# Performance work log

Hardware: AMD Instinct MI355X
Metric: run time of the kernel (lower is better)

The kernel has to match this reference:

```python
import jax, jax.numpy as jnp
import numpy as np

FEATHER = (16, 16)          # in_feather_size
OUT_FEATHER = (16, 16)      # out_feather_size
F = FEATHER[0] * FEATHER[1]            # 256
INNER = (F + 1) ** 2                   # 66049
OUT = OUT_FEATHER[0] * OUT_FEATHER[1]  # 256
B = 2048


def setup_inputs() -> dict:
    key = jax.random.key(0)
    kx, kw, kb = jax.random.split(key, 3)
    x = jax.random.normal(kx, (B, F), dtype=jnp.float32)
    # nn.Linear(INNER, OUT): weight [OUT, INNER], bias [OUT]
    bound = 1.0 / np.sqrt(INNER)
    W = jax.random.uniform(kw, (OUT, INNER), dtype=jnp.float32, minval=-bound, maxval=bound)
    b = jax.random.uniform(kb, (OUT,), dtype=jnp.float32, minval=-bound, maxval=bound)
    return {"x": x, "W": W, "b": b}


def reference(x, W, b):
    # x: [B, F] -> prepend 1 -> x1: [B, F+1]
    x = x.reshape(-1, F)
    ones = jnp.ones((x.shape[0], 1), dtype=x.dtype)
    x1 = jnp.concatenate([ones, x], axis=-1)          # [B, F+1]
    # batched outer product, flattened: [B, (F+1)^2]
    outer = (x1[:, :, None] * x1[:, None, :]).reshape(x.shape[0], INNER)
    y = outer @ W.T + b                               # [B, OUT]
    return y.reshape(-1, OUT_FEATHER[0], OUT_FEATHER[1])
```

## Files before the change

### kernel.cpp

```cpp
#include <hip/hip_runtime.h>
#include <cstdint>
#include <cstddef>


typedef _Float16 half8 __attribute__((ext_vector_type(8)));
typedef float    f32x4 __attribute__((ext_vector_type(4)));

#define KSPLIT 16

#define WAITVM(N) asm volatile("s_waitcnt vmcnt(" #N ")" ::: "memory")
#define WAITLGKM  asm volatile("s_waitcnt lgkmcnt(0)" ::: "memory")

__device__ __forceinline__ void gload_lds16(const void* g, void* lds) {
  __builtin_amdgcn_global_load_lds(
      (const __attribute__((address_space(1))) uint32_t*)g,
      (__attribute__((address_space(3))) uint32_t*)lds, 16, 0, 0);
}

__global__ void conv_w_k(const float* __restrict__ W, _Float16* __restrict__ Wp) {
  int t   = blockIdx.x * 256 + threadIdx.x;
  int j8  = t & 31;
  int rem = t >> 5;
  int ii  = rem % 258;
  int o   = rem / 258;
  float v[8];
  if (ii < 257) {
    const float* src = W + (size_t)o * 66049 + ii * 257 + j8 * 8;
#pragma unroll
    for (int u = 0; u < 8; ++u) v[u] = src[u];
  } else {
    const float* src = W + (size_t)o * 66049 + 256;
#pragma unroll
    for (int u = 0; u < 8; ++u) v[u] = src[(size_t)(j8 * 8 + u) * 257];
  }
  half8 h;
#pragma unroll
  for (int u = 0; u < 8; ++u) h[u] = (_Float16)v[u];
  *(half8*)(Wp + ((size_t)o * 258 + ii) * 256 + j8 * 8) = h;
}

__global__ void conv_x1_k(const float* __restrict__ x, _Float16* __restrict__ X1g) {
  int t  = blockIdx.x * 256 + threadIdx.x;
  int j8 = t % 33;
  int b  = t / 33;
  half8 h;
#pragma unroll
  for (int u = 0; u < 8; ++u) {
    int jj = j8 * 8 + u;
    float v = (jj == 0) ? 1.0f : (jj <= 256 ? x[(size_t)b * 256 + (jj - 1)] : 0.0f);
    h[u] = (_Float16)v;
  }
  *(half8*)(X1g + (size_t)b * 264 + j8 * 8) = h;
}

__global__ void init_out_k(const float* __restrict__ x, const float* __restrict__ W,
                           const float* __restrict__ bias, float* __restrict__ Y) {
  int o = threadIdx.x;
  int b = blockIdx.x;
  float xl = x[(size_t)b * 256 + 255];
  float w  = W[(size_t)o * 66049 + 66048];
  Y[(size_t)b * 256 + o] = bias[o] + xl * xl * w;
}

__global__ __launch_bounds__(512, 2)
void gemm_k(const _Float16* __restrict__ Wp, const _Float16* __restrict__ X1g,
            float* __restrict__ Y) {
  __shared__ __align__(16) _Float16 x1t[128 * 264];
  __shared__ __align__(16) _Float16 wbuf[3 * 8192];

  const int bid = blockIdx.x;
  const int s   = bid & (KSPLIT - 1);
  const int mt  = bid >> 4;
  const int nii = 16 + (s < 2 ? 1 : 0);
  const int ii0 = s * 16 + (s < 2 ? s : 2);

  const int tid = threadIdx.x;
  const int l   = tid & 63;
  const int w   = tid >> 6;
  const int wm  = w >> 2;
  const int wn  = w & 3;
  const int ln  = l & 15;
  const int ks  = l >> 4;

  const _Float16* xsrc = X1g + (size_t)mt * (128 * 264);
  for (int it = 0; it < 9; ++it) {
    int idx = it * 512 + tid;
    if (idx < 4224)
      gload_lds16(xsrc + idx * 8, (char*)x1t + (it * 512 + w * 64) * 16);
  }
  WAITVM(0);
  __builtin_amdgcn_s_barrier();

  half8 base[4][8];
#pragma unroll
  for (int mf = 0; mf < 4; ++mf)
#pragma unroll
    for (int jc = 0; jc < 8; ++jc)
      base[mf][jc] = *(const half8*)(x1t + (wm * 64 + mf * 16 + ln) * 264 + jc * 32 + ks * 8);

  f32x4 acc[4][4];
#pragma unroll
  for (int mf = 0; mf < 4; ++mf)
#pragma unroll
    for (int nf = 0; nf < 4; ++nf) acc[mf][nf] = (f32x4){0.f, 0.f, 0.f, 0.f};

  auto stage = [&](int buf, int ii, int jc) {
#pragma unroll
    for (int t2 = 0; t2 < 2; ++t2) {
      int f = t2 * 8 + w;
      const _Float16* g = Wp + ((size_t)(f * 16 + ln) * 258 + ii) * 256 + jc * 32 + ks * 8;
      gload_lds16(g, (char*)wbuf + buf * 16384 + f * 1024);
    }
  };

  const int nsteps = nii * 8;
  stage(0, ii0, 0);
  stage(1, ii0, 1);
  WAITVM(2);
  __builtin_amdgcn_s_barrier();

  int bc = 0;
  for (int iio = 0; iio < nii; ++iio) {
    const int ii = ii0 + iio;
    const int si = (ii < 257) ? ii : 256;
    half8 s8[4];
#pragma unroll
    for (int mf = 0; mf < 4; ++mf) {
      _Float16 sv = x1t[(wm * 64 + mf * 16 + ln) * 264 + si];
      s8[mf] = (half8){sv, sv, sv, sv, sv, sv, sv, sv};
    }
#pragma unroll
    for (int jc = 0; jc < 8; ++jc) {
      const int st  = iio * 8 + jc;
      const int st2 = st + 2;
      int bs = bc + 2; if (bs >= 3) bs -= 3;
      const bool more = (st2 < nsteps);
      if (more) stage(bs, ii0 + (st2 >> 3), st2 & 7);

      half8 af[4];
#pragma unroll
      for (int mf = 0; mf < 4; ++mf) af[mf] = base[mf][jc] * s8[mf];

      const _Float16* wb = wbuf + bc * 8192 + (wn * 4) * 512 + l * 8;
#pragma unroll
      for (int nf = 0; nf < 4; ++nf) {
        half8 bf = *(const half8*)(wb + nf * 512);
#pragma unroll
        for (int mf = 0; mf < 4; ++mf)
          acc[mf][nf] = __builtin_amdgcn_mfma_f32_16x16x32_f16(af[mf], bf, acc[mf][nf], 0, 0, 0);
      }
      if (more) { WAITVM(2); } else { WAITVM(0); }
      WAITLGKM;
      __builtin_amdgcn_s_barrier();
      bc = bc + 1; if (bc == 3) bc = 0;
    }
  }

  float* yb = Y + (size_t)(mt * 128 + wm * 64) * 256 + wn * 64;
  const int r0 = ks * 4;
#pragma unroll
  for (int mf = 0; mf < 4; ++mf)
#pragma unroll
    for (int nf = 0; nf < 4; ++nf)
#pragma unroll
      for (int r = 0; r < 4; ++r)
        unsafeAtomicAdd(&yb[(size_t)(mf * 16 + r0 + r) * 256 + nf * 16 + ln],
                        acc[mf][nf][r]);
}

__global__ void fb_k(const float* __restrict__ x, const float* __restrict__ W,
                     const float* __restrict__ bias, float* __restrict__ Y) {
  __shared__ float x1[257];
  int b = blockIdx.x, o = threadIdx.x;
  x1[o + 1] = x[(size_t)b * 256 + o];
  if (o == 0) x1[0] = 1.0f;
  __syncthreads();
  const float* Wr = W + (size_t)o * 66049;
  float acc = bias[o];
  for (int i = 0; i < 257; ++i) {
    const float* wr = Wr + (size_t)i * 257;
    float p = 0.f;
    for (int j = 0; j < 257; ++j) p = fmaf(x1[j], wr[j], p);
    acc = fmaf(x1[i], p, acc);
  }
  Y[(size_t)b * 256 + o] = acc;
}

extern "C" void kernel_launch(void* const* d_in, const int* in_sizes, int n_in,
                              void* d_out, int out_size, void* d_ws, size_t ws_size,
                              hipStream_t stream) {
  const float* x = (const float*)d_in[0];
  const float* W = (const float*)d_in[1];
  const float* b = (const float*)d_in[2];
  float* y = (float*)d_out;

  const size_t WPB = (size_t)256 * 258 * 256 * 2;
  const size_t X1B = (size_t)2048 * 264 * 2;
  if (ws_size < WPB + X1B) {
    fb_k<<<2048, 256, 0, stream>>>(x, W, b, y);
    return;
  }
  _Float16* Wp  = (_Float16*)d_ws;
  _Float16* X1g = (_Float16*)((char*)d_ws + WPB);

  conv_w_k<<<8256, 256, 0, stream>>>(W, Wp);
  conv_x1_k<<<264, 256, 0, stream>>>(x, X1g);
  init_out_k<<<2048, 256, 0, stream>>>(x, W, b, y);
  gemm_k<<<256, 512, 0, stream>>>(Wp, X1g, y);
}
```

Before: 156.4 us.

## Drop x1 LDS tile, load base fragments from global, deepen W prefetch to 4 buffers

Removes the 128x264 x1 tile from LDS. Base fragments are now loaded straight from global into registers, and only the per-k-slice scalar column goes into a small LDS array. The freed LDS space allows a 4-slot W ring buffer with prefetch distance 3 instead of 2, which is meant to hide more global latency. It also reduces LDS per block, which could help occupancy, but the uncoalesced global loads for base and the scalars add their own latency.

```diff
diff --git a/kernel.cpp b/kernel.cpp
--- a/kernel.cpp
+++ b/kernel.cpp
@@ -65,8 +65,8 @@
 __global__ __launch_bounds__(512, 2)
 void gemm_k(const _Float16* __restrict__ Wp, const _Float16* __restrict__ X1g,
             float* __restrict__ Y) {
-  __shared__ __align__(16) _Float16 x1t[128 * 264];
-  __shared__ __align__(16) _Float16 wbuf[3 * 8192];
+  __shared__ __align__(16) _Float16 wbuf[4 * 8192];
+  __shared__ _Float16 scal[17 * 128];
 
   const int bid = blockIdx.x;
   const int s   = bid & (KSPLIT - 1);
@@ -82,21 +82,21 @@
   const int ln  = l & 15;
   const int ks  = l >> 4;
 
-  const _Float16* xsrc = X1g + (size_t)mt * (128 * 264);
-  for (int it = 0; it < 9; ++it) {
-    int idx = it * 512 + tid;
-    if (idx < 4224)
-      gload_lds16(xsrc + idx * 8, (char*)x1t + (it * 512 + w * 64) * 16);
-  }
-  WAITVM(0);
-  __builtin_amdgcn_s_barrier();
+  for (int t = tid; t < nii * 128; t += 512) {
+    int k = t >> 7, m = t & 127;
+    int ii = ii0 + k; if (ii > 256) ii = 256;
+    scal[k * 128 + m] = X1g[(size_t)(mt * 128 + m) * 264 + ii];
+  }
 
   half8 base[4][8];
-#pragma unroll
-  for (int mf = 0; mf < 4; ++mf)
-#pragma unroll
-    for (int jc = 0; jc < 8; ++jc)
-      base[mf][jc] = *(const half8*)(x1t + (wm * 64 + mf * 16 + ln) * 264 + jc * 32 + ks * 8);
+  {
+    const _Float16* xr = X1g + (size_t)(mt * 128 + wm * 64 + ln) * 264 + ks * 8;
+#pragma unroll
+    for (int mf = 0; mf < 4; ++mf)
+#pragma unroll
+      for (int jc = 0; jc < 8; ++jc)
+        base[mf][jc] = *(const half8*)(xr + (size_t)mf * (16 * 264) + jc * 32);
+  }
 
   f32x4 acc[4][4];
 #pragma unroll
@@ -116,32 +116,29 @@
   const int nsteps = nii * 8;
   stage(0, ii0, 0);
   stage(1, ii0, 1);
-  WAITVM(2);
+  stage(2, ii0, 2);
+  WAITVM(4);
+  WAITLGKM;
   __builtin_amdgcn_s_barrier();
 
-  int bc = 0;
   for (int iio = 0; iio < nii; ++iio) {
-    const int ii = ii0 + iio;
-    const int si = (ii < 257) ? ii : 256;
     half8 s8[4];
 #pragma unroll
     for (int mf = 0; mf < 4; ++mf) {
-      _Float16 sv = x1t[(wm * 64 + mf * 16 + ln) * 264 + si];
+      _Float16 sv = scal[iio * 128 + wm * 64 + mf * 16 + ln];
       s8[mf] = (half8){sv, sv, sv, sv, sv, sv, sv, sv};
     }
 #pragma unroll
     for (int jc = 0; jc < 8; ++jc) {
       const int st  = iio * 8 + jc;
-      const int st2 = st + 2;
-      int bs = bc + 2; if (bs >= 3) bs -= 3;
-      const bool more = (st2 < nsteps);
-      if (more) stage(bs, ii0 + (st2 >> 3), st2 & 7);
+      const int st3 = st + 3;
+      if (st3 < nsteps) stage(st3 & 3, ii0 + (st3 >> 3), st3 & 7);
 
       half8 af[4];
 #pragma unroll
       for (int mf = 0; mf < 4; ++mf) af[mf] = base[mf][jc] * s8[mf];
 
-      const _Float16* wb = wbuf + bc * 8192 + (wn * 4) * 512 + l * 8;
+      const _Float16* wb = wbuf + (st & 3) * 8192 + (wn * 4) * 512 + l * 8;
 #pragma unroll
       for (int nf = 0; nf < 4; ++nf) {
         half8 bf = *(const half8*)(wb + nf * 512);
@@ -149,10 +146,12 @@
         for (int mf = 0; mf < 4; ++mf)
           acc[mf][nf] = __builtin_amdgcn_mfma_f32_16x16x32_f16(af[mf], bf, acc[mf][nf], 0, 0, 0);
       }
-      if (more) { WAITVM(2); } else { WAITVM(0); }
+      const int rem = nsteps - 1 - st;
+      if (rem >= 3)      { WAITVM(4); }
+      else if (rem == 2) { WAITVM(2); }
+      else if (rem == 1) { WAITVM(0); }
       WAITLGKM;
       __builtin_amdgcn_s_barrier();
-      bc = bc + 1; if (bc == 3) bc = 0;
     }
   }
 
```

New measurement: 142.9 us. 1.09x faster.
